# Performance work log

Measured on AMD Instinct MI355X. Metric: run time of the kernel, lower is better.

## Reference

```python
import jax, jax.numpy as jnp
import numpy as np

N = 65536      # flattened latent vectors (e.g. 64 images x 32x32 latents)
K = 1024       # num_embeddings (codebook size)
D = 64         # latent_dim


def setup_inputs() -> dict:
    key = jax.random.key(0)
    k_x, k_e = jax.random.split(key)
    inputs = jax.random.normal(k_x, (N, D), dtype=jnp.float32)
    # codebook initialized ~ tf.random_normal_initializer (stddev=0.05)
    embeddings = jax.random.normal(k_e, (K, D), dtype=jnp.float32) * 0.05
    return {"inputs": inputs, "embeddings": embeddings}


def reference(inputs, embeddings):
    # Pairwise L2 distances ||x_n - e_k||_2 -> [N, K].
    x_sq = jnp.sum(inputs * inputs, axis=-1, keepdims=True)        # [N, 1]
    e_sq = jnp.sum(embeddings * embeddings, axis=-1)               # [K]
    cross = inputs @ embeddings.T                                   # [N, K]
    sq_dist = x_sq + e_sq[None, :] - 2.0 * cross                    # [N, K]
    return jnp.sqrt(jnp.maximum(sq_dist, 0.0))
```

## Files before the change

kernel.cpp:

```cpp
#include <hip/hip_runtime.h>


typedef __attribute__((ext_vector_type(8))) short short8;
typedef __attribute__((ext_vector_type(4))) float floatx4;

#define LSTR 72
#define N_ROWS 65536

__device__ __forceinline__ unsigned short f2bf(float f) {
    unsigned int u = __float_as_uint(f);
    u += 0x7FFFu + ((u >> 16) & 1u);
    return (unsigned short)(u >> 16);
}
__device__ __forceinline__ float bf2f(unsigned short h) {
    return __uint_as_float(((unsigned int)h) << 16);
}

__global__ __launch_bounds__(256, 4) void vq_fused(const float* __restrict__ X,
                                                   const float* __restrict__ E,
                                                   float* __restrict__ out,
                                                   int Ktot) {
    __shared__ alignas(16) unsigned short lds[2 * 128 * LSTR];
    __shared__ alignas(16) float s_xsq[128];
    __shared__ alignas(16) float s_esq[128];

    const int tid = threadIdx.x;

    const int nxb = Ktot >> 7;
    const int cpx = gridDim.x >> 3;
    const int bid = blockIdx.x;
    const int swz = (bid & 7) * cpx + (bid >> 3);
    const int bx = swz % nxb;
    const int by = swz / nxb;
    const size_t m0 = (size_t)by * 128;
    const int n0 = bx * 128;

    unsigned short* ldsA = lds;
    unsigned short* ldsB = lds + 128 * LSTR;

    const float* gX = X + m0 * 64;
    const float* gE = E + (size_t)n0 * 64;

    #pragma unroll
    for (int half = 0; half < 2; ++half) {
        const float* g = half ? gE : gX;
        unsigned short* dst = half ? ldsB : ldsA;
        float* sq = half ? s_esq : s_xsq;
        float4 v[4][2];
        #pragma unroll
        for (int it = 0; it < 4; ++it) {
            const int gg = it * 256 + tid;
            const int row = gg >> 3, c8 = (gg & 7) * 8;
            const float* p = g + row * 64 + c8;
            v[it][0] = *(const float4*)p;
            v[it][1] = *(const float4*)(p + 4);
        }
        #pragma unroll
        for (int it = 0; it < 4; ++it) {
            const int gg = it * 256 + tid;
            const int row = gg >> 3, c8 = (gg & 7) * 8;
            const float* f = (const float*)&v[it][0];
            float s = 0.f;
            short8 pk;
            #pragma unroll
            for (int j = 0; j < 8; ++j) {
                const unsigned short h = f2bf(f[j]);
                const float r = bf2f(h);
                s = fmaf(r, r, s);
                pk[j] = (short)h;
            }
            *(short8*)&dst[row * LSTR + c8] = pk;
            s += __shfl_down(s, 4, 8);
            s += __shfl_down(s, 2, 8);
            s += __shfl_down(s, 1, 8);
            if ((tid & 7) == 0) sq[row] = s;
        }
    }
    __syncthreads();

    const int w = tid >> 6;
    const int lane = tid & 63;
    const int quad = lane >> 4;
    const int l16 = lane & 15;
    const int wm = (w >> 1) * 64;
    const int wn = (w & 1) * 64;

    short8 b0[4], b1[4];
    #pragma unroll
    for (int t = 0; t < 4; ++t) {
        const int br = wn + t * 16 + l16;
        b0[t] = *(const short8*)&ldsB[br * LSTR + quad * 8];
        b1[t] = *(const short8*)&ldsB[br * LSTR + 32 + quad * 8];
    }

    #pragma unroll
    for (int i = 0; i < 4; ++i) {
        const int ar = wm + i * 16 + l16;
        const short8 a0 = *(const short8*)&ldsA[ar * LSTR + quad * 8];
        const short8 a1 = *(const short8*)&ldsA[ar * LSTR + 32 + quad * 8];

        floatx4 acc[4];
        #pragma unroll
        for (int j = 0; j < 4; ++j) {
            acc[j] = __builtin_amdgcn_mfma_f32_16x16x32_bf16(
                b0[j], a0, (floatx4){0.f, 0.f, 0.f, 0.f}, 0, 0, 0);
            acc[j] = __builtin_amdgcn_mfma_f32_16x16x32_bf16(
                b1[j], a1, acc[j], 0, 0, 0);
        }

        const int orow = wm + i * 16 + l16;
        const float xq = s_xsq[orow];
        float* op = out + (m0 + orow) * (size_t)Ktot + n0;
        #pragma unroll
        for (int j = 0; j < 4; ++j) {
            const int ncol0 = wn + j * 16 + quad * 4;
            const floatx4 eqv = *(const floatx4*)&s_esq[ncol0];
            const floatx4 c = acc[j];
            floatx4 o;
            #pragma unroll
            for (int r = 0; r < 4; ++r)
                o[r] = __builtin_amdgcn_sqrtf(fmaxf(xq + eqv[r] - 2.0f * c[r], 0.0f));
            *(floatx4*)(op + ncol0) = o;
        }
    }
}

extern "C" void kernel_launch(void* const* d_in, const int* in_sizes, int n_in,
                              void* d_out, int out_size, void* d_ws, size_t ws_size,
                              hipStream_t stream) {
    const float* X = (const float*)d_in[0];
    const float* E = (const float*)d_in[1];
    float* out = (float*)d_out;
    const int K = in_sizes[1] / 64;

    const int tiles = (N_ROWS / 128) * (K / 128);
    vq_fused<<<dim3(tiles), dim3(256), 0, stream>>>(X, E, out, K);
}
```

Before: 280.5 us.

## Load MFMA fragments directly from global memory, dropping LDS staging and barrier

```diff
diff --git a/kernel.cpp b/kernel.cpp
--- a/kernel.cpp
+++ b/kernel.cpp
@@ -4,7 +4,6 @@
 typedef __attribute__((ext_vector_type(8))) short short8;
 typedef __attribute__((ext_vector_type(4))) float floatx4;
 
-#define LSTR 72
 #define N_ROWS 65536
 
 __device__ __forceinline__ unsigned short f2bf(float f) {
@@ -16,14 +15,21 @@
     return __uint_as_float(((unsigned int)h) << 16);
 }
 
+__device__ __forceinline__ void cvt8(float4 lo, float4 hi, short8* frag, float* s) {
+    const float f[8] = {lo.x, lo.y, lo.z, lo.w, hi.x, hi.y, hi.z, hi.w};
+    #pragma unroll
+    for (int k = 0; k < 8; ++k) {
+        const unsigned short h = f2bf(f[k]);
+        const float r = bf2f(h);
+        *s = fmaf(r, r, *s);
+        (*frag)[k] = (short)h;
+    }
+}
+
 __global__ __launch_bounds__(256, 4) void vq_fused(const float* __restrict__ X,
                                                    const float* __restrict__ E,
                                                    float* __restrict__ out,
                                                    int Ktot) {
-    __shared__ alignas(16) unsigned short lds[2 * 128 * LSTR];
-    __shared__ alignas(16) float s_xsq[128];
-    __shared__ alignas(16) float s_esq[128];
-
     const int tid = threadIdx.x;
 
     const int nxb = Ktot >> 7;
@@ -35,49 +41,6 @@
     const size_t m0 = (size_t)by * 128;
     const int n0 = bx * 128;
 
-    unsigned short* ldsA = lds;
-    unsigned short* ldsB = lds + 128 * LSTR;
-
-    const float* gX = X + m0 * 64;
-    const float* gE = E + (size_t)n0 * 64;
-
-    #pragma unroll
-    for (int half = 0; half < 2; ++half) {
-        const float* g = half ? gE : gX;
-        unsigned short* dst = half ? ldsB : ldsA;
-        float* sq = half ? s_esq : s_xsq;
-        float4 v[4][2];
-        #pragma unroll
-        for (int it = 0; it < 4; ++it) {
-            const int gg = it * 256 + tid;
-            const int row = gg >> 3, c8 = (gg & 7) * 8;
-            const float* p = g + row * 64 + c8;
-            v[it][0] = *(const float4*)p;
-            v[it][1] = *(const float4*)(p + 4);
-        }
-        #pragma unroll
-        for (int it = 0; it < 4; ++it) {
-            const int gg = it * 256 + tid;
-            const int row = gg >> 3, c8 = (gg & 7) * 8;
-            const float* f = (const float*)&v[it][0];
-            float s = 0.f;
-            short8 pk;
-            #pragma unroll
-            for (int j = 0; j < 8; ++j) {
-                const unsigned short h = f2bf(f[j]);
-                const float r = bf2f(h);
-                s = fmaf(r, r, s);
-                pk[j] = (short)h;
-            }
-            *(short8*)&dst[row * LSTR + c8] = pk;
-            s += __shfl_down(s, 4, 8);
-            s += __shfl_down(s, 2, 8);
-            s += __shfl_down(s, 1, 8);
-            if ((tid & 7) == 0) sq[row] = s;
-        }
-    }
-    __syncthreads();
-
     const int w = tid >> 6;
     const int lane = tid & 63;
     const int quad = lane >> 4;
@@ -86,18 +49,45 @@
     const int wn = (w & 1) * 64;
 
     short8 b0[4], b1[4];
-    #pragma unroll
-    for (int t = 0; t < 4; ++t) {
-        const int br = wn + t * 16 + l16;
-        b0[t] = *(const short8*)&ldsB[br * LSTR + quad * 8];
-        b1[t] = *(const short8*)&ldsB[br * LSTR + 32 + quad * 8];
+    floatx4 eq[4];
+    {
+        float en[4];
+        #pragma unroll
+        for (int t = 0; t < 4; ++t) {
+            const float* er = E + (size_t)(n0 + wn + t * 16 + l16) * 64 + quad * 8;
+            const float4 e0 = *(const float4*)er;
+            const float4 e1 = *(const float4*)(er + 4);
+            const float4 e2 = *(const float4*)(er + 32);
+            const float4 e3 = *(const float4*)(er + 36);
+            float s = 0.f;
+            cvt8(e0, e1, &b0[t], &s);
+            cvt8(e2, e3, &b1[t], &s);
+            s += __shfl_xor(s, 16, 64);
+            s += __shfl_xor(s, 32, 64);
+            en[t] = s;
+        }
+        #pragma unroll
+        for (int j = 0; j < 4; ++j)
+            #pragma unroll
+            for (int r = 0; r < 4; ++r)
+                eq[j][r] = __shfl(en[j], quad * 4 + r, 64);
     }
 
     #pragma unroll
     for (int i = 0; i < 4; ++i) {
-        const int ar = wm + i * 16 + l16;
-        const short8 a0 = *(const short8*)&ldsA[ar * LSTR + quad * 8];
-        const short8 a1 = *(const short8*)&ldsA[ar * LSTR + 32 + quad * 8];
+        const int orow = wm + i * 16 + l16;
+        const float* xr = X + (m0 + orow) * 64 + quad * 8;
+        const float4 x0 = *(const float4*)xr;
+        const float4 x1 = *(const float4*)(xr + 4);
+        const float4 x2 = *(const float4*)(xr + 32);
+        const float4 x3 = *(const float4*)(xr + 36);
+        short8 a0, a1;
+        float s = 0.f;
+        cvt8(x0, x1, &a0, &s);
+        cvt8(x2, x3, &a1, &s);
+        s += __shfl_xor(s, 16, 64);
+        s += __shfl_xor(s, 32, 64);
+        const float xq = s;
 
         floatx4 acc[4];
         #pragma unroll
@@ -108,18 +98,16 @@
                 b1[j], a1, acc[j], 0, 0, 0);
         }
 
-        const int orow = wm + i * 16 + l16;
-        const float xq = s_xsq[orow];
         float* op = out + (m0 + orow) * (size_t)Ktot + n0;
         #pragma unroll
         for (int j = 0; j < 4; ++j) {
             const int ncol0 = wn + j * 16 + quad * 4;
-            const floatx4 eqv = *(const floatx4*)&s_esq[ncol0];
             const floatx4 c = acc[j];
+            const floatx4 e = eq[j];
             floatx4 o;
             #pragma unroll
             for (int r = 0; r < 4; ++r)
-                o[r] = __builtin_amdgcn_sqrtf(fmaxf(xq + eqv[r] - 2.0f * c[r], 0.0f));
+                o[r] = __builtin_amdgcn_sqrtf(fmaxf(xq + e[r] - 2.0f * c[r], 0.0f));
             *(floatx4*)(op + ncol0) = o;
         }
     }
```

Result: slower. 322.7 us (+15.0%).

## Make each block own a row strip and loop over codebook tiles with prefetch

Applied to the files above, without the earlier changes.

```diff
diff --git a/kernel.cpp b/kernel.cpp
--- a/kernel.cpp
+++ b/kernel.cpp
@@ -16,50 +16,43 @@
     return __uint_as_float(((unsigned int)h) << 16);
 }
 
-__global__ __launch_bounds__(256, 4) void vq_fused(const float* __restrict__ X,
+__global__ __launch_bounds__(256, 2) void vq_fused(const float* __restrict__ X,
                                                    const float* __restrict__ E,
                                                    float* __restrict__ out,
                                                    int Ktot) {
-    __shared__ alignas(16) unsigned short lds[2 * 128 * LSTR];
+    __shared__ alignas(16) unsigned short ldsX[128 * LSTR];
+    __shared__ alignas(16) unsigned short ldsE[128 * LSTR];
     __shared__ alignas(16) float s_xsq[128];
     __shared__ alignas(16) float s_esq[128];
 
     const int tid = threadIdx.x;
 
-    const int nxb = Ktot >> 7;
     const int cpx = gridDim.x >> 3;
     const int bid = blockIdx.x;
-    const int swz = (bid & 7) * cpx + (bid >> 3);
-    const int bx = swz % nxb;
-    const int by = swz / nxb;
-    const size_t m0 = (size_t)by * 128;
-    const int n0 = bx * 128;
+    const size_t m0 = (size_t)((bid & 7) * cpx + (bid >> 3)) * 128;
 
-    unsigned short* ldsA = lds;
-    unsigned short* ldsB = lds + 128 * LSTR;
+    const int srow = tid >> 3;
+    const int sc8 = (tid & 7) * 8;
 
-    const float* gX = X + m0 * 64;
-    const float* gE = E + (size_t)n0 * 64;
-
+    float4 vx[4][2], ve[4][2];
+    #pragma unroll
+    for (int it = 0; it < 4; ++it) {
+        const int row = it * 32 + srow;
+        const float* p = X + (m0 + row) * 64 + sc8;
+        vx[it][0] = *(const float4*)p;
+        vx[it][1] = *(const float4*)(p + 4);
+        const float* q = E + (size_t)row * 64 + sc8;
+        ve[it][0] = *(const float4*)q;
+        ve[it][1] = *(const float4*)(q + 4);
+    }
     #pragma unroll
     for (int half = 0; half < 2; ++half) {
-        const float* g = half ? gE : gX;
-        unsigned short* dst = half ? ldsB : ldsA;
+        unsigned short* dst = half ? ldsE : ldsX;
         float* sq = half ? s_esq : s_xsq;
-        float4 v[4][2];
         #pragma unroll
         for (int it = 0; it < 4; ++it) {
-            const int gg = it * 256 + tid;
-            const int row = gg >> 3, c8 = (gg & 7) * 8;
-            const float* p = g + row * 64 + c8;
-            v[it][0] = *(const float4*)p;
-            v[it][1] = *(const float4*)(p + 4);
-        }
-        #pragma unroll
-        for (int it = 0; it < 4; ++it) {
-            const int gg = it * 256 + tid;
-            const int row = gg >> 3, c8 = (gg & 7) * 8;
-            const float* f = (const float*)&v[it][0];
+            const int row = it * 32 + srow;
+            const float* f = half ? (const float*)&ve[it][0] : (const float*)&vx[it][0];
             float s = 0.f;
             short8 pk;
             #pragma unroll
@@ -69,7 +62,7 @@
                 s = fmaf(r, r, s);
                 pk[j] = (short)h;
             }
-            *(short8*)&dst[row * LSTR + c8] = pk;
+            *(short8*)&dst[row * LSTR + sc8] = pk;
             s += __shfl_down(s, 4, 8);
             s += __shfl_down(s, 2, 8);
             s += __shfl_down(s, 1, 8);
@@ -85,42 +78,88 @@
     const int wm = (w >> 1) * 64;
     const int wn = (w & 1) * 64;
 
-    short8 b0[4], b1[4];
-    #pragma unroll
-    for (int t = 0; t < 4; ++t) {
-        const int br = wn + t * 16 + l16;
-        b0[t] = *(const short8*)&ldsB[br * LSTR + quad * 8];
-        b1[t] = *(const short8*)&ldsB[br * LSTR + 32 + quad * 8];
-    }
-
+    short8 xa0[4], xa1[4];
+    float xqv[4];
     #pragma unroll
     for (int i = 0; i < 4; ++i) {
         const int ar = wm + i * 16 + l16;
-        const short8 a0 = *(const short8*)&ldsA[ar * LSTR + quad * 8];
-        const short8 a1 = *(const short8*)&ldsA[ar * LSTR + 32 + quad * 8];
+        xa0[i] = *(const short8*)&ldsX[ar * LSTR + quad * 8];
+        xa1[i] = *(const short8*)&ldsX[ar * LSTR + 32 + quad * 8];
+        xqv[i] = s_xsq[ar];
+    }
 
-        floatx4 acc[4];
+    for (int jt = 0; jt < 8; ++jt) {
+        const int n0 = jt * 128;
+
+        short8 b0[4], b1[4];
+        floatx4 eqv[4];
         #pragma unroll
-        for (int j = 0; j < 4; ++j) {
-            acc[j] = __builtin_amdgcn_mfma_f32_16x16x32_bf16(
-                b0[j], a0, (floatx4){0.f, 0.f, 0.f, 0.f}, 0, 0, 0);
-            acc[j] = __builtin_amdgcn_mfma_f32_16x16x32_bf16(
-                b1[j], a1, acc[j], 0, 0, 0);
+        for (int t = 0; t < 4; ++t) {
+            const int br = wn + t * 16 + l16;
+            b0[t] = *(const short8*)&ldsE[br * LSTR + quad * 8];
+            b1[t] = *(const short8*)&ldsE[br * LSTR + 32 + quad * 8];
+            eqv[t] = *(const floatx4*)&s_esq[wn + t * 16 + quad * 4];
         }
 
-        const int orow = wm + i * 16 + l16;
-        const float xq = s_xsq[orow];
-        float* op = out + (m0 + orow) * (size_t)Ktot + n0;
+        float4 pf[4][2];
+        if (jt < 7) {
+            const float* gEn = E + (size_t)(n0 + 128) * 64;
+            #pragma unroll
+            for (int it = 0; it < 4; ++it) {
+                const float* q = gEn + (it * 32 + srow) * 64 + sc8;
+                pf[it][0] = *(const float4*)q;
+                pf[it][1] = *(const float4*)(q + 4);
+            }
+        }
+
         #pragma unroll
-        for (int j = 0; j < 4; ++j) {
-            const int ncol0 = wn + j * 16 + quad * 4;
-            const floatx4 eqv = *(const floatx4*)&s_esq[ncol0];
-            const floatx4 c = acc[j];
-            floatx4 o;
+        for (int i = 0; i < 4; ++i) {
+            floatx4 acc[4];
             #pragma unroll
-            for (int r = 0; r < 4; ++r)
-                o[r] = __builtin_amdgcn_sqrtf(fmaxf(xq + eqv[r] - 2.0f * c[r], 0.0f));
-            *(floatx4*)(op + ncol0) = o;
+            for (int j = 0; j < 4; ++j) {
+                acc[j] = __builtin_amdgcn_mfma_f32_16x16x32_bf16(
+                    b0[j], xa0[i], (floatx4){0.f, 0.f, 0.f, 0.f}, 0, 0, 0);
+                acc[j] = __builtin_amdgcn_mfma_f32_16x16x32_bf16(
+                    b1[j], xa1[i], acc[j], 0, 0, 0);
+            }
+            const int orow = wm + i * 16 + l16;
+            const float xq = xqv[i];
+            float* op = out + (m0 + orow) * (size_t)Ktot + n0;
+            #pragma unroll
+            for (int j = 0; j < 4; ++j) {
+                const int ncol0 = wn + j * 16 + quad * 4;
+                const floatx4 c = acc[j];
+                const floatx4 e = eqv[j];
+                floatx4 o;
+                #pragma unroll
+                for (int r = 0; r < 4; ++r)
+                    o[r] = __builtin_amdgcn_sqrtf(fmaxf(xq + e[r] - 2.0f * c[r], 0.0f));
+                *(floatx4*)(op + ncol0) = o;
+            }
+        }
+
+        if (jt < 7) {
+            __syncthreads();
+            #pragma unroll
+            for (int it = 0; it < 4; ++it) {
+                const int row = it * 32 + srow;
+                const float* f = (const float*)&pf[it][0];
+                float s = 0.f;
+                short8 pk;
+                #pragma unroll
+                for (int j = 0; j < 8; ++j) {
+                    const unsigned short h = f2bf(f[j]);
+                    const float r = bf2f(h);
+                    s = fmaf(r, r, s);
+                    pk[j] = (short)h;
+                }
+                *(short8*)&ldsE[row * LSTR + sc8] = pk;
+                s += __shfl_down(s, 4, 8);
+                s += __shfl_down(s, 2, 8);
+                s += __shfl_down(s, 1, 8);
+                if ((tid & 7) == 0) s_esq[row] = s;
+            }
+            __syncthreads();
         }
     }
 }
@@ -133,6 +172,5 @@
     float* out = (float*)d_out;
     const int K = in_sizes[1] / 64;
 
-    const int tiles = (N_ROWS / 128) * (K / 128);
-    vq_fused<<<dim3(tiles), dim3(256), 0, stream>>>(X, E, out, K);
+    vq_fused<<<dim3(N_ROWS / 128), dim3(256), 0, stream>>>(X, E, out, K);
 }
```

New measurement: 294.8 us. 5.1% more time.
